# Performance work log

Measured on AMD Instinct MI355X. Metric: run time of the kernel, lower is better.

Reference implementation:

```python
import jax, jax.numpy as jnp
import numpy as np

Z, N, K, W = 131072, 64, 64, 32


def setup_inputs() -> dict:
    key = jax.random.key(0)
    k1, k2, k3 = jax.random.split(key, 3)
    features = jax.random.normal(k1, (Z, N), dtype=jnp.float32)
    # dense realization of the CG-derived mixing tensor 'wkij'
    mixing_matrix = jax.random.normal(k2, (W, K, N, N), dtype=jnp.float32) * 0.05
    weight = jax.random.normal(k3, (W,), dtype=jnp.float32)
    return {"features": features, "mixing_matrix": mixing_matrix, "weight": weight}


def reference(features, mixing_matrix, weight):
    # torch: einsum('w,wkij,zi,zj->zk', weight, mixing_matrix, features, features)
    # Contract the small path axis w first -> [K, N, N] (cheap, tiny output),
    # then the bilinear square over z. einsum chooses a GEMM-style path; the
    # [Z, N, N] outer-product side is the memory-bound part.
    M = jnp.einsum('w,wkij->kij', weight, mixing_matrix)  # [K, N, N]
    out = jnp.einsum('kij,zi,zj->zk', M, features, features)  # [Z, K]
    return out
```

## Files before the change

kernel.cpp:

```cpp
#include <hip/hip_runtime.h>
#include <stdint.h>

typedef __attribute__((ext_vector_type(8))) _Float16 half8;
typedef __attribute__((ext_vector_type(2))) _Float16 h2;
typedef __attribute__((ext_vector_type(4))) float f32x4;

static __device__ __forceinline__ unsigned short f2h(float f) {
  return __builtin_bit_cast(unsigned short, (_Float16)f);
}

__global__ __launch_bounds__(1024) void prep_kernel(const float* __restrict__ mix,
                                                    const float* __restrict__ wgt,
                                                    unsigned short* __restrict__ Bp) {
  __shared__ float T[4096];
  const int k   = blockIdx.x;
  const int tid = threadIdx.x;
  const float4* m4 = (const float4*)mix + (size_t)k * 1024 + tid;
  float4 a = {0.f, 0.f, 0.f, 0.f};
#pragma unroll
  for (int w = 0; w < 32; ++w) {
    const float s = wgt[w];
    const float4 v = m4[(size_t)w * 65536];
    a.x += s * v.x; a.y += s * v.y; a.z += s * v.z; a.w += s * v.w;
  }
  *(float4*)(&T[tid * 4]) = a;
  __syncthreads();
  ushort4 r;
#pragma unroll
  for (int e = 0; e < 4; ++e) {
    const int t = tid * 4 + e, i = t >> 6, j = t & 63;
    float v;
    if (i < j)       v = T[t] + T[(j << 6) | i];
    else if (i == j) v = T[t];
    else             v = 0.f;
    ((unsigned short*)&r)[e] = f2h(v);
  }
  const int t0  = tid * 4;
  const int off = ((t0 >> 5) * 4 + (k >> 4)) * 512 + ((t0 >> 3) & 3) * 128
                + (k & 15) * 8 + (t0 & 7);
  *(ushort4*)(Bp + off) = r;
}

static __device__ __forceinline__ void blk_coords(int idx, int& c, int& il, int& h) {
  if (idx < 64) { c = idx >> 2; il = (idx >> 1) & 1; h = idx & 1; }
  else { const int r = idx - 64; c = 16 + (r >> 1); il = r & 1; h = 1; }
}

__global__ __launch_bounds__(256, 3) void gemm_kernel(const float* __restrict__ X,
                                                      const unsigned short* __restrict__ Bp,
                                                      float* __restrict__ out) {
  const int tid  = threadIdx.x;
  const int lane = tid & 63;
  const int wv   = tid >> 6;
  const int m    = lane & 15;
  const int q    = lane >> 4;
  const int zblk = blockIdx.x * 128;

  h2 jh[2][8];
  {
    const float4* X4g = (const float4*)X;
#pragma unroll
    for (int f = 0; f < 2; ++f) {
      const int zg = zblk + wv * 32 + f * 16 + m;
#pragma unroll
      for (int h = 0; h < 2; ++h) {
        const float4 a = X4g[zg * 16 + h * 8 + q * 2];
        const float4 b = X4g[zg * 16 + h * 8 + q * 2 + 1];
        jh[f][h * 4 + 0] = h2{(_Float16)a.x, (_Float16)a.y};
        jh[f][h * 4 + 1] = h2{(_Float16)a.z, (_Float16)a.w};
        jh[f][h * 4 + 2] = h2{(_Float16)b.x, (_Float16)b.y};
        jh[f][h * 4 + 3] = h2{(_Float16)b.z, (_Float16)b.w};
      }
    }
  }

  f32x4 acc[2][4];
#pragma unroll
  for (int f = 0; f < 2; ++f)
#pragma unroll
    for (int g = 0; g < 4; ++g) acc[f][g] = f32x4{0.f, 0.f, 0.f, 0.f};

  const uint4* Bv = (const uint4*)Bp;
  uint4 bbuf[3][4];
  auto loadB = [&](int idx, uint4* dst) {
    int c, il, h; blk_coords(idx, c, il, h);
    const int s4 = (c * 4 + il * 2 + h) * 4;
#pragma unroll
    for (int g = 0; g < 4; ++g) dst[g] = Bv[(s4 + g) * 64 + lane];
  };

  loadB(0, bbuf[0]);
  loadB(1, bbuf[1]);

#pragma unroll
  for (int idx = 0; idx < 96; ++idx) {
    if (idx + 2 < 96) loadB(idx + 2, bbuf[(idx + 2) % 3]);

    int c, il, h; blk_coords(idx, c, il, h);
    const int i    = 2 * c + il;
    const int hs   = i >> 5;
    const int qs   = (i >> 3) & 3;
    const int es   = (i & 7) >> 1;
    const int half = i & 1;
    h2 s2f[2];
#pragma unroll
    for (int f = 0; f < 2; ++f) {
      const int du = __shfl((int)__builtin_bit_cast(unsigned, jh[f][hs * 4 + es]),
                            qs * 16 + m, 64);
      const unsigned uu = (unsigned)du;
      s2f[f] = __builtin_bit_cast(h2, __builtin_amdgcn_perm(uu, uu,
                                   half ? 0x03020302u : 0x01000100u));
    }

    const uint4* bc = bbuf[idx % 3];
#pragma unroll
    for (int f = 0; f < 2; ++f) {
      union { unsigned u[4]; half8 v; } A;
#pragma unroll
      for (int e = 0; e < 4; ++e) {
        const h2 pr = s2f[f] * jh[f][h * 4 + e];
        A.u[e] = __builtin_bit_cast(unsigned, pr);
      }
#pragma unroll
      for (int g = 0; g < 4; ++g)
        acc[f][g] = __builtin_amdgcn_mfma_f32_16x16x32_f16(
            A.v, __builtin_bit_cast(half8, bc[g]), acc[f][g], 0, 0, 0);
    }
  }

#pragma unroll
  for (int f = 0; f < 2; ++f) {
    const int zr = zblk + wv * 32 + f * 16 + q * 4;
#pragma unroll
    for (int g = 0; g < 4; ++g)
#pragma unroll
      for (int r = 0; r < 4; ++r)
        out[(size_t)(zr + r) * 64 + g * 16 + m] = acc[f][g][r];
  }
}

extern "C" void kernel_launch(void* const* d_in, const int* in_sizes, int n_in,
                              void* d_out, int out_size, void* d_ws, size_t ws_size,
                              hipStream_t stream) {
  const float* X   = (const float*)d_in[0];
  const float* mix = (const float*)d_in[1];
  const float* wgt = (const float*)d_in[2];
  float* out = (float*)d_out;
  unsigned short* Bp = (unsigned short*)d_ws;

  prep_kernel<<<64, 1024, 0, stream>>>(mix, wgt, Bp);
  gemm_kernel<<<1024, 256, 0, stream>>>(X, Bp, out);
}
```

Measured before the change: 158.6 us.

## Stage mixing matrix through LDS and enlarge per-wave z tile

The GEMM kernel now processes 256 rows per block, and each wave covers 128 z rows by 32 output k columns. It stages the symmetric B matrix into swizzled, double-buffered LDS with global_load_lds instead of loading it from global memory into registers for every block of 32 rows. Each B fragment is reused across 8 row tiles instead of 2, which is meant to cut redundant B traffic. In exchange it uses many more registers (jh[8][8], acc[8][2]), lowers occupancy to 2 blocks, and relies on hand-written waitcnt synchronisation with no barrier between waves.

```diff
diff --git a/kernel.cpp b/kernel.cpp
--- a/kernel.cpp
+++ b/kernel.cpp
@@ -7,6 +7,10 @@
 
 static __device__ __forceinline__ unsigned short f2h(float f) {
   return __builtin_bit_cast(unsigned short, (_Float16)f);
+}
+static __device__ __forceinline__ void gload16(const void* g, void* l) {
+  __builtin_amdgcn_global_load_lds((const __attribute__((address_space(1))) void*)g,
+                                   (__attribute__((address_space(3))) void*)l, 16, 0, 0);
 }
 
 __global__ __launch_bounds__(1024) void prep_kernel(const float* __restrict__ mix,
@@ -35,33 +39,29 @@
     else             v = 0.f;
     ((unsigned short*)&r)[e] = f2h(v);
   }
-  const int t0  = tid * 4;
-  const int off = ((t0 >> 5) * 4 + (k >> 4)) * 512 + ((t0 >> 3) & 3) * 128
-                + (k & 15) * 8 + (t0 & 7);
-  *(ushort4*)(Bp + off) = r;
+  ((ushort4*)Bp)[k * 1024 + tid] = r;
 }
 
-static __device__ __forceinline__ void blk_coords(int idx, int& c, int& il, int& h) {
-  if (idx < 64) { c = idx >> 2; il = (idx >> 1) & 1; h = idx & 1; }
-  else { const int r = idx - 64; c = 16 + (r >> 1); il = r & 1; h = 1; }
-}
-
-__global__ __launch_bounds__(256, 3) void gemm_kernel(const float* __restrict__ X,
+__global__ __launch_bounds__(256, 2) void gemm_kernel(const float* __restrict__ X,
                                                       const unsigned short* __restrict__ Bp,
                                                       float* __restrict__ out) {
+  __shared__ unsigned short ldsB[4][2][4096];
+
   const int tid  = threadIdx.x;
   const int lane = tid & 63;
   const int wv   = tid >> 6;
+  const int wzg  = wv >> 1;
+  const int wk   = wv & 1;
   const int m    = lane & 15;
   const int q    = lane >> 4;
-  const int zblk = blockIdx.x * 128;
+  const int zblk = blockIdx.x * 256;
 
-  h2 jh[2][8];
+  h2 jh[8][8];
   {
     const float4* X4g = (const float4*)X;
 #pragma unroll
-    for (int f = 0; f < 2; ++f) {
-      const int zg = zblk + wv * 32 + f * 16 + m;
+    for (int f = 0; f < 8; ++f) {
+      const int zg = zblk + wzg * 128 + f * 16 + m;
 #pragma unroll
       for (int h = 0; h < 2; ++h) {
         const float4 a = X4g[zg * 16 + h * 8 + q * 2];
@@ -74,68 +74,87 @@
     }
   }
 
-  f32x4 acc[2][4];
+  f32x4 acc[8][2];
 #pragma unroll
-  for (int f = 0; f < 2; ++f)
+  for (int f = 0; f < 8; ++f) {
+    acc[f][0] = f32x4{0.f, 0.f, 0.f, 0.f};
+    acc[f][1] = f32x4{0.f, 0.f, 0.f, 0.f};
+  }
+
+  asm volatile("s_waitcnt vmcnt(0)" ::: "memory");
+
+  const unsigned short* gB = Bp + (size_t)(wk * 32) * 4096;
+  unsigned short* myB = &ldsB[wv][0][0];
+
+  auto stageB = [&](int ct, int bf) {
 #pragma unroll
-    for (int g = 0; g < 4; ++g) acc[f][g] = f32x4{0.f, 0.f, 0.f, 0.f};
-
-  const uint4* Bv = (const uint4*)Bp;
-  uint4 bbuf[3][4];
-  auto loadB = [&](int idx, uint4* dst) {
-    int c, il, h; blk_coords(idx, c, il, h);
-    const int s4 = (c * 4 + il * 2 + h) * 4;
-#pragma unroll
-    for (int g = 0; g < 4; ++g) dst[g] = Bv[(s4 + g) * 64 + lane];
+    for (int s = 0; s < 8; ++s) {
+      const int row = s * 4 + (lane >> 4);
+      const int u   = (lane & 15) ^ (row & 15);
+      gload16(gB + (size_t)row * 4096 + ct * 128 + u * 8,
+              myB + bf * 4096 + s * 512);
+    }
   };
 
-  loadB(0, bbuf[0]);
-  loadB(1, bbuf[1]);
+  stageB(0, 0);
+  stageB(1, 1);
 
 #pragma unroll
-  for (int idx = 0; idx < 96; ++idx) {
-    if (idx + 2 < 96) loadB(idx + 2, bbuf[(idx + 2) % 3]);
+  for (int hs = 0; hs < 2; ++hs) {
+#pragma unroll 1
+    for (int qs = 0; qs < 4; ++qs) {
+#pragma unroll
+      for (int es = 0; es < 4; ++es) {
+        const int c = hs * 16 + qs * 4 + es;
+        asm volatile("s_waitcnt vmcnt(8)" ::: "memory");
 
-    int c, il, h; blk_coords(idx, c, il, h);
-    const int i    = 2 * c + il;
-    const int hs   = i >> 5;
-    const int qs   = (i >> 3) & 3;
-    const int es   = (i & 7) >> 1;
-    const int half = i & 1;
-    h2 s2f[2];
+        const unsigned short* Bl = myB + (es & 1) * 4096;
 #pragma unroll
-    for (int f = 0; f < 2; ++f) {
-      const int du = __shfl((int)__builtin_bit_cast(unsigned, jh[f][hs * 4 + es]),
-                            qs * 16 + m, 64);
-      const unsigned uu = (unsigned)du;
-      s2f[f] = __builtin_bit_cast(h2, __builtin_amdgcn_perm(uu, uu,
-                                   half ? 0x03020302u : 0x01000100u));
-    }
-
-    const uint4* bc = bbuf[idx % 3];
+        for (int il = 0; il < 2; ++il) {
+          h2 s2f[8];
 #pragma unroll
-    for (int f = 0; f < 2; ++f) {
-      union { unsigned u[4]; half8 v; } A;
+          for (int f = 0; f < 8; ++f) {
+            const int du = __shfl((int)__builtin_bit_cast(unsigned, jh[f][hs * 4 + es]),
+                                  qs * 16 + m, 64);
+            const unsigned uu = (unsigned)du;
+            s2f[f] = __builtin_bit_cast(h2, __builtin_amdgcn_perm(uu, uu,
+                                     il ? 0x03020302u : 0x01000100u));
+          }
 #pragma unroll
-      for (int e = 0; e < 4; ++e) {
-        const h2 pr = s2f[f] * jh[f][h * 4 + e];
-        A.u[e] = __builtin_bit_cast(unsigned, pr);
+          for (int h = 0; h < 2; ++h) {
+            if (hs == 1 && h == 0) continue;
+            const int sb = il * 2 + h;
+            const int u  = (sb * 4 + q) ^ m;
+            const unsigned short* bb = Bl + m * 128 + u * 8;
+            const half8 b0 = *(const half8*)(const void*)(bb);
+            const half8 b1 = *(const half8*)(const void*)(bb + 16 * 128);
+#pragma unroll
+            for (int f = 0; f < 8; ++f) {
+              union { unsigned u[4]; half8 v; } A;
+#pragma unroll
+              for (int e = 0; e < 4; ++e) {
+                const h2 pr = s2f[f] * jh[f][h * 4 + e];
+                A.u[e] = __builtin_bit_cast(unsigned, pr);
+              }
+              acc[f][0] = __builtin_amdgcn_mfma_f32_16x16x32_f16(A.v, b0, acc[f][0], 0, 0, 0);
+              acc[f][1] = __builtin_amdgcn_mfma_f32_16x16x32_f16(A.v, b1, acc[f][1], 0, 0, 0);
+            }
+          }
+        }
+        asm volatile("s_waitcnt lgkmcnt(0)" ::: "memory");
+        stageB((c + 2) & 31, es & 1);
       }
-#pragma unroll
-      for (int g = 0; g < 4; ++g)
-        acc[f][g] = __builtin_amdgcn_mfma_f32_16x16x32_f16(
-            A.v, __builtin_bit_cast(half8, bc[g]), acc[f][g], 0, 0, 0);
     }
   }
 
 #pragma unroll
-  for (int f = 0; f < 2; ++f) {
-    const int zr = zblk + wv * 32 + f * 16 + q * 4;
+  for (int f = 0; f < 8; ++f) {
+    const int zr = zblk + wzg * 128 + f * 16 + q * 4;
 #pragma unroll
-    for (int g = 0; g < 4; ++g)
+    for (int g = 0; g < 2; ++g)
 #pragma unroll
       for (int r = 0; r < 4; ++r)
-        out[(size_t)(zr + r) * 64 + g * 16 + m] = acc[f][g][r];
+        out[(size_t)(zr + r) * 64 + wk * 32 + g * 16 + m] = acc[f][g][r];
   }
 }
 
@@ -149,5 +168,5 @@
   unsigned short* Bp = (unsigned short*)d_ws;
 
   prep_kernel<<<64, 1024, 0, stream>>>(mix, wgt, Bp);
-  gemm_kernel<<<1024, 256, 0, stream>>>(X, Bp, out);
+  gemm_kernel<<<512, 256, 0, stream>>>(X, Bp, out);
 }
```

New measurement: 148.5 us. 1.07x faster.
